# Optimization experiments

Measured on AMD Instinct MI355X. Metric: run time of the kernel, lower is better.

The kernel has to match this reference:

```python
import jax, jax.numpy as jnp
import numpy as np

EPS = 1e-05

def setup_inputs() -> dict:
    key = jax.random.key(0)
    inputs = jax.random.normal(key, (32, 512, 768), dtype=jnp.float32)
    return {"inputs": inputs}

def reference(inputs) -> jnp.ndarray:
    # position weight: L2 norm per token, w[b,l] = sqrt(1e-5 + sum_d x^2)
    w = jnp.sqrt(EPS + jnp.sum(inputs * inputs, axis=-1))  # [B, L]
    # output[b,d,e] = sum_l w[b,l] * x[b,l,d] * x[b,l,e]
    # fused weighted Gram matrix; never materializes [B,L,D,D]
    return jnp.einsum('bld,ble->bde', inputs * w[..., None], inputs)
```

## Files before the change

kernel.cpp:

```cpp
#include <hip/hip_runtime.h>
#include <hip/hip_bf16.h>

#define BATCH 32
#define LL 512
#define DD 768
#define EPSC 1e-5f

typedef __attribute__((ext_vector_type(8))) short bf16x8;
typedef __attribute__((ext_vector_type(4))) float f32x4;

__global__ __launch_bounds__(256) void k_scales(const float* __restrict__ x,
                                                float* __restrict__ s) {
    int wave = threadIdx.x >> 6;
    int lane = threadIdx.x & 63;
    int row = blockIdx.x * 4 + wave;
    const float4* xr = (const float4*)(x + (size_t)row * DD);
    float sum = 0.f;
#pragma unroll
    for (int i = 0; i < 3; i++) {
        float4 v = xr[lane + i * 64];
        sum += v.x * v.x + v.y * v.y + v.z * v.z + v.w * v.w;
    }
#pragma unroll
    for (int off = 32; off > 0; off >>= 1)
        sum += __shfl_xor(sum, off, 64);
    if (lane == 0) s[row] = sqrtf(sqrtf(EPSC + sum));
}

__global__ __launch_bounds__(256) void k_transpose(const float* __restrict__ x,
                                                   const float* __restrict__ s,
                                                   __hip_bfloat16* __restrict__ yt) {
    __shared__ float tile[64][65];
    __shared__ float svec[64];
    int b = blockIdx.z;
    int l0 = blockIdx.y * 64;
    int d0 = blockIdx.x * 64;
    int tx = threadIdx.x & 63;
    int ty = threadIdx.x >> 6;
    const float* xp = x + ((size_t)b * LL + l0) * DD + d0;
#pragma unroll
    for (int i = 0; i < 16; i++) {
        int r = ty * 16 + i;
        tile[r][tx] = xp[(size_t)r * DD + tx];
    }
    if (threadIdx.x < 64) svec[threadIdx.x] = s[b * LL + l0 + threadIdx.x];
    __syncthreads();
    __hip_bfloat16* yp = yt + ((size_t)b * DD + d0) * LL + l0;
#pragma unroll
    for (int i = 0; i < 16; i++) {
        int r = ty * 16 + i;
        float v = tile[tx][r] * svec[tx];
        yp[(size_t)r * LL + tx] = __float2bfloat16(v);
    }
}

__global__ __launch_bounds__(256) void k_gemm(const ushort* __restrict__ yt,
                                              float* __restrict__ out) {
    __shared__ ushort At[128 * 32];
    __shared__ ushort Bt[128 * 32];
    int b = blockIdx.y;
    int tm = blockIdx.x / 6, tn = blockIdx.x % 6;
    int m0 = tm * 128, n0 = tn * 128;
    int tid = threadIdx.x;
    int wave = tid >> 6, lane = tid & 63;
    int wr = wave >> 1, wc = wave & 1;
    const ushort* yb = yt + (size_t)b * DD * LL;

    f32x4 acc[4][4];
#pragma unroll
    for (int i = 0; i < 4; i++)
#pragma unroll
        for (int j = 0; j < 4; j++) acc[i][j] = (f32x4){0.f, 0.f, 0.f, 0.f};

    int srow = lane >> 2;
    int scol = (lane & 3) * 8;

    for (int ks = 0; ks < 16; ks++) {
        int k0 = ks * 32;
        __syncthreads();
#pragma unroll
        for (int i = 0; i < 2; i++) {
            int rloc = wave * 32 + i * 16 + srow;
            const ushort* gA = yb + (size_t)(m0 + rloc) * LL + k0 + scol;
            const ushort* gB = yb + (size_t)(n0 + rloc) * LL + k0 + scol;
            __builtin_amdgcn_global_load_lds(
                (const __attribute__((address_space(1))) void*)gA,
                (__attribute__((address_space(3))) void*)(At + (wave * 32 + i * 16) * 32),
                16, 0, 0);
            __builtin_amdgcn_global_load_lds(
                (const __attribute__((address_space(1))) void*)gB,
                (__attribute__((address_space(3))) void*)(Bt + (wave * 32 + i * 16) * 32),
                16, 0, 0);
        }
        __syncthreads();

        bf16x8 afrag[4], bfrag[4];
#pragma unroll
        for (int i = 0; i < 4; i++) {
            int m = wr * 64 + i * 16 + (lane & 15);
            afrag[i] = *(const bf16x8*)(At + m * 32 + (lane >> 4) * 8);
            int n = wc * 64 + i * 16 + (lane & 15);
            bfrag[i] = *(const bf16x8*)(Bt + n * 32 + (lane >> 4) * 8);
        }
#pragma unroll
        for (int i = 0; i < 4; i++)
#pragma unroll
            for (int j = 0; j < 4; j++)
                acc[i][j] = __builtin_amdgcn_mfma_f32_16x16x32_bf16(
                    afrag[i], bfrag[j], acc[i][j], 0, 0, 0);
    }

    float* op = out + (size_t)b * DD * DD;
#pragma unroll
    for (int i = 0; i < 4; i++) {
        int mbase = m0 + wr * 64 + i * 16 + (lane >> 4) * 4;
#pragma unroll
        for (int j = 0; j < 4; j++) {
            int n = n0 + wc * 64 + j * 16 + (lane & 15);
#pragma unroll
            for (int r = 0; r < 4; r++)
                op[(size_t)(mbase + r) * DD + n] = acc[i][j][r];
        }
    }
}

extern "C" void kernel_launch(void* const* d_in, const int* in_sizes, int n_in,
                              void* d_out, int out_size, void* d_ws, size_t ws_size,
                              hipStream_t stream) {
    const float* x = (const float*)d_in[0];
    float* s = (float*)d_ws;
    __hip_bfloat16* yt = (__hip_bfloat16*)((char*)d_ws + 65536);

    k_scales<<<dim3((BATCH * LL) / 4), 256, 0, stream>>>(x, s);
    k_transpose<<<dim3(DD / 64, LL / 64, BATCH), 256, 0, stream>>>(x, s, yt);
    k_gemm<<<dim3(36, BATCH), 256, 0, stream>>>((const ushort*)yt, (float*)d_out);
}
```

Measured before the change: 155.9 us.

## Exploit Gram symmetry: compute upper-triangle tiles, mirror writes, vectorize transpose

The GEMM now launches only the 21 upper-triangular 128x128 tiles per batch, using 21 rather than 36 blocks. Each off-diagonal tile writes both itself and its mirrored transpose, and diagonal tiles reuse the A tile in LDS as B. Blocks are mapped so each batch stays on one XCD for L2 locality. The transpose kernel switches to float4 loads and 16-byte bf16x8 stores. This roughly cuts MFMA work by 40%, at the cost of uneven per-block write volume and strided scalar stores for the mirrored half.

Measured after the change: 142.8 us. -8.4%, faster.

```diff
diff --git a/kernel.cpp b/kernel.cpp
--- a/kernel.cpp
+++ b/kernel.cpp
@@ -29,28 +29,37 @@
 
 __global__ __launch_bounds__(256) void k_transpose(const float* __restrict__ x,
                                                    const float* __restrict__ s,
-                                                   __hip_bfloat16* __restrict__ yt) {
-    __shared__ float tile[64][65];
+                                                   ushort* __restrict__ yt) {
+    __shared__ float tile[64][68];
     __shared__ float svec[64];
     int b = blockIdx.z;
     int l0 = blockIdx.y * 64;
     int d0 = blockIdx.x * 64;
-    int tx = threadIdx.x & 63;
-    int ty = threadIdx.x >> 6;
+    int t = threadIdx.x;
+    if (t < 64) svec[t] = s[b * LL + l0 + t];
     const float* xp = x + ((size_t)b * LL + l0) * DD + d0;
+    int c4 = (t & 15) * 4, lr = t >> 4;
 #pragma unroll
-    for (int i = 0; i < 16; i++) {
-        int r = ty * 16 + i;
-        tile[r][tx] = xp[(size_t)r * DD + tx];
+    for (int r = 0; r < 4; r++) {
+        int l = lr + r * 16;
+        float4 v = *(const float4*)(xp + (size_t)l * DD + c4);
+        *(float4*)&tile[l][c4] = v;
     }
-    if (threadIdx.x < 64) svec[threadIdx.x] = s[b * LL + l0 + threadIdx.x];
     __syncthreads();
-    __hip_bfloat16* yp = yt + ((size_t)b * DD + d0) * LL + l0;
+    ushort* yp = yt + ((size_t)b * DD + d0) * LL + l0;
+    int lc = t & 7, dl0 = t >> 3;
 #pragma unroll
-    for (int i = 0; i < 16; i++) {
-        int r = ty * 16 + i;
-        float v = tile[tx][r] * svec[tx];
-        yp[(size_t)r * LL + tx] = __float2bfloat16(v);
+    for (int it = 0; it < 2; it++) {
+        int dl = dl0 + it * 32;
+        bf16x8 w;
+#pragma unroll
+        for (int j = 0; j < 8; j++) {
+            int l = lc * 8 + j;
+            float v = tile[l][dl] * svec[l];
+            __hip_bfloat16 h = __float2bfloat16(v);
+            w[j] = *(short*)&h;
+        }
+        *(bf16x8*)(yp + (size_t)dl * LL + lc * 8) = w;
     }
 }
 
@@ -58,8 +67,14 @@
                                               float* __restrict__ out) {
     __shared__ ushort At[128 * 32];
     __shared__ ushort Bt[128 * 32];
-    int b = blockIdx.y;
-    int tm = blockIdx.x / 6, tn = blockIdx.x % 6;
+    int i = blockIdx.x;
+    int xcd = i & 7, slot = i >> 3;
+    int b = xcd + 8 * (slot / 21);
+    int p = slot % 21;
+    int t = p, tm = 0, rem = 6;
+    while (t >= rem) { t -= rem; rem--; tm++; }
+    int tn = tm + t;
+    bool diag = (tm == tn);
     int m0 = tm * 128, n0 = tn * 128;
     int tid = threadIdx.x;
     int wave = tid >> 6, lane = tid & 63;
@@ -68,9 +83,9 @@
 
     f32x4 acc[4][4];
 #pragma unroll
-    for (int i = 0; i < 4; i++)
+    for (int ii = 0; ii < 4; ii++)
 #pragma unroll
-        for (int j = 0; j < 4; j++) acc[i][j] = (f32x4){0.f, 0.f, 0.f, 0.f};
+        for (int j = 0; j < 4; j++) acc[ii][j] = (f32x4){0.f, 0.f, 0.f, 0.f};
 
     int srow = lane >> 2;
     int scol = (lane & 3) * 8;
@@ -79,47 +94,62 @@
         int k0 = ks * 32;
         __syncthreads();
 #pragma unroll
-        for (int i = 0; i < 2; i++) {
-            int rloc = wave * 32 + i * 16 + srow;
+        for (int c = 0; c < 2; c++) {
+            int rloc = wave * 32 + c * 16 + srow;
             const ushort* gA = yb + (size_t)(m0 + rloc) * LL + k0 + scol;
-            const ushort* gB = yb + (size_t)(n0 + rloc) * LL + k0 + scol;
             __builtin_amdgcn_global_load_lds(
                 (const __attribute__((address_space(1))) void*)gA,
-                (__attribute__((address_space(3))) void*)(At + (wave * 32 + i * 16) * 32),
+                (__attribute__((address_space(3))) void*)(At + (wave * 32 + c * 16) * 32),
                 16, 0, 0);
-            __builtin_amdgcn_global_load_lds(
-                (const __attribute__((address_space(1))) void*)gB,
-                (__attribute__((address_space(3))) void*)(Bt + (wave * 32 + i * 16) * 32),
-                16, 0, 0);
+            if (!diag) {
+                const ushort* gB = yb + (size_t)(n0 + rloc) * LL + k0 + scol;
+                __builtin_amdgcn_global_load_lds(
+                    (const __attribute__((address_space(1))) void*)gB,
+                    (__attribute__((address_space(3))) void*)(Bt + (wave * 32 + c * 16) * 32),
+                    16, 0, 0);
+            }
         }
         __syncthreads();
 
+        const ushort* Bsrc = diag ? At : Bt;
         bf16x8 afrag[4], bfrag[4];
 #pragma unroll
-        for (int i = 0; i < 4; i++) {
-            int m = wr * 64 + i * 16 + (lane & 15);
-            afrag[i] = *(const bf16x8*)(At + m * 32 + (lane >> 4) * 8);
-            int n = wc * 64 + i * 16 + (lane & 15);
-            bfrag[i] = *(const bf16x8*)(Bt + n * 32 + (lane >> 4) * 8);
+        for (int ii = 0; ii < 4; ii++) {
+            int m = wr * 64 + ii * 16 + (lane & 15);
+            afrag[ii] = *(const bf16x8*)(At + m * 32 + (lane >> 4) * 8);
+            int n = wc * 64 + ii * 16 + (lane & 15);
+            bfrag[ii] = *(const bf16x8*)(Bsrc + n * 32 + (lane >> 4) * 8);
         }
 #pragma unroll
-        for (int i = 0; i < 4; i++)
+        for (int ii = 0; ii < 4; ii++)
 #pragma unroll
             for (int j = 0; j < 4; j++)
-                acc[i][j] = __builtin_amdgcn_mfma_f32_16x16x32_bf16(
-                    afrag[i], bfrag[j], acc[i][j], 0, 0, 0);
+                acc[ii][j] = __builtin_amdgcn_mfma_f32_16x16x32_bf16(
+                    afrag[ii], bfrag[j], acc[ii][j], 0, 0, 0);
     }
 
     float* op = out + (size_t)b * DD * DD;
 #pragma unroll
-    for (int i = 0; i < 4; i++) {
-        int mbase = m0 + wr * 64 + i * 16 + (lane >> 4) * 4;
+    for (int ii = 0; ii < 4; ii++) {
+        int colb = m0 + wr * 64 + ii * 16 + (lane >> 4) * 4;
 #pragma unroll
         for (int j = 0; j < 4; j++) {
-            int n = n0 + wc * 64 + j * 16 + (lane & 15);
+            int row = n0 + wc * 64 + j * 16 + (lane & 15);
+            float4 v = {acc[ii][j][0], acc[ii][j][1], acc[ii][j][2], acc[ii][j][3]};
+            *(float4*)(op + (size_t)row * DD + colb) = v;
+        }
+    }
+    if (!diag) {
 #pragma unroll
-            for (int r = 0; r < 4; r++)
-                op[(size_t)(mbase + r) * DD + n] = acc[i][j][r];
+        for (int ii = 0; ii < 4; ii++) {
+            int mbase = m0 + wr * 64 + ii * 16 + (lane >> 4) * 4;
+#pragma unroll
+            for (int j = 0; j < 4; j++) {
+                int n = n0 + wc * 64 + j * 16 + (lane & 15);
+#pragma unroll
+                for (int r = 0; r < 4; r++)
+                    op[(size_t)(mbase + r) * DD + n] = acc[ii][j][r];
+            }
         }
     }
 }
@@ -129,9 +159,9 @@
                               hipStream_t stream) {
     const float* x = (const float*)d_in[0];
     float* s = (float*)d_ws;
-    __hip_bfloat16* yt = (__hip_bfloat16*)((char*)d_ws + 65536);
+    ushort* yt = (ushort*)((char*)d_ws + 65536);
 
     k_scales<<<dim3((BATCH * LL) / 4), 256, 0, stream>>>(x, s);
     k_transpose<<<dim3(DD / 64, LL / 64, BATCH), 256, 0, stream>>>(x, s, yt);
-    k_gemm<<<dim3(36, BATCH), 256, 0, stream>>>((const ushort*)yt, (float*)d_out);
+    k_gemm<<<dim3(21 * BATCH), 256, 0, stream>>>(yt, (float*)d_out);
 }
```
